# Kernel optimization log

Hardware: AMD Instinct MI355X
Metric: run time of the kernel (lower is better)

Reference implementation:

```python
import jax, jax.numpy as jnp
import numpy as np

B, T, C, H = 2, 2048, 1024, 16
D = C // H  # head_dim = 64


def setup_inputs() -> dict:
    key = jax.random.key(0)
    ks = jax.random.split(key, 5)
    s = 1.0 / np.sqrt(C)
    return {
        "x": jax.random.normal(ks[0], (B, T, C), jnp.float32),
        "Wq": jax.random.normal(ks[1], (C, C), jnp.float32) * s,
        "bq": jnp.zeros((C,), jnp.float32),
        "Wk": jax.random.normal(ks[2], (C, C), jnp.float32) * s,
        "bk": jnp.zeros((C,), jnp.float32),
        "Wv": jax.random.normal(ks[3], (C, C), jnp.float32) * s,
        "bv": jnp.zeros((C,), jnp.float32),
        "Wo": jax.random.normal(ks[4], (C, C), jnp.float32) * s,
        "bo": jnp.zeros((C,), jnp.float32),
    }


def reference(x, Wq, bq, Wk, bk, Wv, bv, Wo, bo):
    Bx, Tx, Cx = x.shape
    # torch Linear: y = x @ W.T + b
    q = (x @ Wq.T + bq).reshape(Bx, Tx, H, D).transpose(0, 2, 1, 3)  # [B,H,T,D]
    k = (x @ Wk.T + bk).reshape(Bx, Tx, H, D).transpose(0, 2, 1, 3)
    v = (x @ Wv.T + bv).reshape(Bx, Tx, H, D).transpose(0, 2, 1, 3)
    att = jnp.einsum("bhqd,bhkd->bhqk", q, k) / np.sqrt(D).astype(np.float32)
    mask = jnp.tril(jnp.ones((Tx, Tx), bool))  # causal mask [T,T]
    att = jnp.where(mask, att, -jnp.inf)
    att = jax.nn.softmax(att, axis=-1)
    out = jnp.einsum("bhqk,bhkd->bhqd", att, v)
    out = out.transpose(0, 2, 1, 3).reshape(Bx, Tx, Cx)
    return out @ Wo.T + bo
```

## Files before the change

kernel.cpp:

```cpp
#include <hip/hip_runtime.h>
#include <hip/hip_bf16.h>

#define B_ 2
#define T_ 2048
#define C_ 1024
#define H_ 16
#define D_ 64

typedef unsigned short u16;
typedef __bf16 bf16x8 __attribute__((ext_vector_type(8)));
typedef float floatx4 __attribute__((ext_vector_type(4)));

__device__ __forceinline__ float bf2f(u16 u) {
  union { unsigned int i; float f; } x; x.i = ((unsigned int)u) << 16; return x.f;
}
__device__ __forceinline__ u16 f2bf(float f) {
  union { float f; unsigned int i; } x; x.f = f;
  unsigned int r = x.i + 0x7fffu + ((x.i >> 16) & 1u);
  return (u16)(r >> 16);
}

__device__ __forceinline__ void gld16(void* lds, const void* g) {
  __builtin_amdgcn_global_load_lds(
      (const __attribute__((address_space(1))) unsigned int*)g,
      (__attribute__((address_space(3))) unsigned int*)lds, 16, 0, 0);
}

#define NXF4 1048576
#define NWF4 262144

__global__ __launch_bounds__(256) void cvt_all(
    const float* __restrict__ x,  const float* __restrict__ Wq,
    const float* __restrict__ Wk, const float* __restrict__ Wv,
    const float* __restrict__ Wo, u16* __restrict__ dst_base)
{
  const int i = blockIdx.x * 256 + threadIdx.x;
  const float* src; size_t off;
  if (i < NXF4)               { src = x;  off = i; }
  else if (i < NXF4 + NWF4)   { src = Wq; off = i - NXF4; }
  else if (i < NXF4 + 2*NWF4) { src = Wk; off = i - (NXF4 + NWF4); }
  else if (i < NXF4 + 3*NWF4) { src = Wv; off = i - (NXF4 + 2*NWF4); }
  else                        { src = Wo; off = i - (NXF4 + 3*NWF4); }
  float4 f = ((const float4*)src)[off];
  ushort4 o;
  o.x = f2bf(f.x); o.y = f2bf(f.y); o.z = f2bf(f.z); o.w = f2bf(f.w);
  ((ushort4*)dst_base)[i] = o;
}

#define QSCALE 0.1803368801111f

__global__ __launch_bounds__(256) void gemm_qkv(
    const u16* __restrict__ X, const u16* __restrict__ Wb,
    const float* __restrict__ b0, const float* __restrict__ b1,
    const float* __restrict__ b2,
    u16* __restrict__ Yq, u16* __restrict__ Yk, u16* __restrict__ Yv)
{
  const int K = C_;
  __shared__ __align__(16) u16 As[128 * 32];
  __shared__ __align__(16) u16 Bs[128 * 32];
  __shared__ __align__(16) u16 Es[64 * 128];

  const int tid  = threadIdx.x;
  const int wv   = tid >> 6;
  const int lane = tid & 63;
  const int mcol = lane & 15;
  const int quad = lane >> 4;
  const int wr = wv >> 1, wc = wv & 1;
  const int m0 = blockIdx.x * 128;
  const int n0 = blockIdx.y * 128;
  const int z  = blockIdx.z;

  const u16* W = Wb + (size_t)z * C_ * C_;
  const float* bias = (z == 0 ? b0 : z == 1 ? b1 : b2);

  const int srow = tid >> 2;
  const int scol = (tid & 3) * 8;
  const u16* xp0 = X + (size_t)(m0 + srow) * K + scol;
  const u16* xp1 = xp0 + (size_t)64 * K;
  const u16* wp0 = W + (size_t)(n0 + srow) * K + scol;
  const u16* wp1 = wp0 + (size_t)64 * K;

  floatx4 acc[4][4] = {};

  for (int k0 = 0; k0 < K; k0 += 32) {
    gld16(&As[tid * 8],        xp0 + k0);
    gld16(&As[2048 + tid * 8], xp1 + k0);
    gld16(&Bs[tid * 8],        wp0 + k0);
    gld16(&Bs[2048 + tid * 8], wp1 + k0);
    __syncthreads();

    bf16x8 a[4], b[4];
#pragma unroll
    for (int rf = 0; rf < 4; ++rf)
      a[rf] = *(const bf16x8*)&As[(wr * 64 + rf * 16 + mcol) * 32 + quad * 8];
#pragma unroll
    for (int cf = 0; cf < 4; ++cf)
      b[cf] = *(const bf16x8*)&Bs[(wc * 64 + cf * 16 + mcol) * 32 + quad * 8];
#pragma unroll
    for (int rf = 0; rf < 4; ++rf)
#pragma unroll
      for (int cf = 0; cf < 4; ++cf)
        acc[rf][cf] = __builtin_amdgcn_mfma_f32_16x16x32_bf16(
            a[rf], b[cf], acc[rf][cf], 0, 0, 0);
    __syncthreads();
  }

  if (z == 2) {
#pragma unroll
    for (int p = 0; p < 2; ++p) {
      __syncthreads();
      if (wc == p) {
#pragma unroll
        for (int cf = 0; cf < 4; ++cf) {
          const int rn = cf * 16 + mcol;
          const float bv = b2[n0 + p * 64 + rn];
#pragma unroll
          for (int rf = 0; rf < 4; ++rf) {
            const int gm = wr * 8 + rf * 2 + (quad >> 1);
            const int slot = gm ^ (rn & 7);
            ushort4 pk;
            pk.x = f2bf(acc[rf][cf][0] + bv);
            pk.y = f2bf(acc[rf][cf][1] + bv);
            pk.z = f2bf(acc[rf][cf][2] + bv);
            pk.w = f2bf(acc[rf][cf][3] + bv);
            *(ushort4*)&Es[rn * 128 + slot * 8 + (quad & 1) * 4] = pk;
          }
        }
      }
      __syncthreads();
      const int c = tid & 15;
      const int bb = m0 >> 11;
      const int t0 = (m0 & (T_ - 1)) + c * 8;
#pragma unroll
      for (int i = 0; i < 4; ++i) {
        const int rn = (tid >> 4) + i * 16;
        const int slot = c ^ (rn & 7);
        const uint4 val = *(const uint4*)&Es[rn * 128 + slot * 8];
        const int n = n0 + p * 64 + rn;
        const int h = n >> 6, d = n & (D_ - 1);
        *(uint4*)&Yv[(((size_t)bb * H_ + h) * D_ + d) * T_ + t0] = val;
      }
    }
  } else {
#pragma unroll
    for (int cf = 0; cf < 4; ++cf) {
      const int n = n0 + wc * 64 + cf * 16 + mcol;
      const float bv = bias[n];
      const int h = n >> 6, d = n & (D_ - 1);
#pragma unroll
      for (int rf = 0; rf < 4; ++rf) {
#pragma unroll
        for (int r = 0; r < 4; ++r) {
          const int m = m0 + wr * 64 + rf * 16 + quad * 4 + r;
          const int bb = m >> 11, t = m & (T_ - 1);
          const float v = acc[rf][cf][r] + bv;
          const size_t idx = (((size_t)bb * H_ + h) * T_ + t) * D_ + d;
          if (z == 0) Yq[idx] = f2bf(v * QSCALE);
          else        Yk[idx] = f2bf(v);
        }
      }
    }
  }
}

__global__ __launch_bounds__(256) void gemm_out(
    const u16* __restrict__ X, const u16* __restrict__ W,
    const float* __restrict__ bias, float* __restrict__ Yf)
{
  const int K = C_, N = C_;
  __shared__ __align__(16) u16 As[128 * 32];
  __shared__ __align__(16) u16 Bs[64 * 32];

  const int tid  = threadIdx.x;
  const int wv   = tid >> 6;
  const int lane = tid & 63;
  const int mcol = lane & 15;
  const int quad = lane >> 4;
  const int wr = wv >> 1, wc = wv & 1;
  const int m0 = blockIdx.x * 128;
  const int n0 = blockIdx.y * 64;

  const int srow = tid >> 2;
  const int scol = (tid & 3) * 8;
  const u16* xp0 = X + (size_t)(m0 + srow) * K + scol;
  const u16* xp1 = xp0 + (size_t)64 * K;
  const u16* wp  = W + (size_t)(n0 + srow) * K + scol;

  floatx4 acc[4][2] = {};

  for (int k0 = 0; k0 < K; k0 += 32) {
    gld16(&As[tid * 8],        xp0 + k0);
    gld16(&As[2048 + tid * 8], xp1 + k0);
    gld16(&Bs[tid * 8],        wp + k0);
    __syncthreads();

    bf16x8 a[4], b[2];
#pragma unroll
    for (int rf = 0; rf < 4; ++rf)
      a[rf] = *(const bf16x8*)&As[(wr * 64 + rf * 16 + mcol) * 32 + quad * 8];
#pragma unroll
    for (int cf = 0; cf < 2; ++cf)
      b[cf] = *(const bf16x8*)&Bs[(wc * 32 + cf * 16 + mcol) * 32 + quad * 8];
#pragma unroll
    for (int rf = 0; rf < 4; ++rf)
#pragma unroll
      for (int cf = 0; cf < 2; ++cf)
        acc[rf][cf] = __builtin_amdgcn_mfma_f32_16x16x32_bf16(
            a[rf], b[cf], acc[rf][cf], 0, 0, 0);
    __syncthreads();
  }

#pragma unroll
  for (int cf = 0; cf < 2; ++cf) {
    const int n = n0 + wc * 32 + cf * 16 + mcol;
    const float bv = bias[n];
#pragma unroll
    for (int rf = 0; rf < 4; ++rf) {
#pragma unroll
      for (int r = 0; r < 4; ++r) {
        const int m = m0 + wr * 64 + rf * 16 + quad * 4 + r;
        Yf[(size_t)m * N + n] = acc[rf][cf][r] + bv;
      }
    }
  }
}

__global__ __launch_bounds__(256) void attn_flash(
    const u16* __restrict__ Q, const u16* __restrict__ K,
    const u16* __restrict__ Vg, u16* __restrict__ O)
{
  __shared__ __align__(16) u16 Ks[64 * 64];
  __shared__ __align__(16) u16 Vt[80 * 64];
  __shared__ __align__(16) u16 Ps[4][16 * 72];

  const int tid  = threadIdx.x;
  const int wv   = tid >> 6;
  const int lane = tid & 63;
  const int mcol = lane & 15;
  const int quad = lane >> 4;

  const int bh = blockIdx.x & 31;
  const int pp = blockIdx.x >> 5;
  const size_t base = (size_t)bh * T_ * D_;
  const int b = bh >> 4, h = bh & (H_ - 1);

  for (int idx = tid; idx < 16 * 64; idx += 256)
    Vt[64 * 64 + idx] = (idx < 64) ? (u16)0x3F80 : (u16)0;

  const int srow = lane >> 3;
  const int sg   = (lane & 7) ^ srow;
  const int c0 = wv * 2, c1 = wv * 2 + 1;
  const int sl0 = (quad ^ (mcol & 7)) * 8;

  const int h3 = mcol >> 3, lo = mcol & 7;
  u16* psw = &Ps[wv][0];
  int colsw[4];
#pragma unroll
  for (int nt = 0; nt < 4; ++nt)
    colsw[nt] = (((nt * 2 + h3) ^ quad) * 8) + lo;
  const int g0 = quad ^ (mcol >> 2);

  for (int half = 0; half < 2; ++half) {
    const int iq = half ? (31 - pp) : pp;

    const u16* qg = Q + base + (size_t)(iq * 64 + wv * 16 + mcol) * D_ + quad * 8;
    const bf16x8 qf0 = *(const bf16x8*)qg;
    const bf16x8 qf1 = *(const bf16x8*)(qg + 32);

    floatx4 oacc[5] = {};

    for (int j = 0; j <= iq; ++j) {
      __syncthreads();
      gld16(&Ks[c0 * 512 + lane * 8],
            K + base + (size_t)(j * 64 + c0 * 8 + srow) * D_ + sg * 8);
      gld16(&Ks[c1 * 512 + lane * 8],
            K + base + (size_t)(j * 64 + c1 * 8 + srow) * D_ + sg * 8);
      gld16(&Vt[c0 * 512 + lane * 8],
            Vg + (size_t)bh * D_ * T_ + (size_t)(c0 * 8 + srow) * T_ + j * 64 + sg * 8);
      gld16(&Vt[c1 * 512 + lane * 8],
            Vg + (size_t)bh * D_ * T_ + (size_t)(c1 * 8 + srow) * T_ + j * 64 + sg * 8);
      __syncthreads();

      floatx4 sacc[4] = {};
#pragma unroll
      for (int nt = 0; nt < 4; ++nt) {
        const u16* kr = &Ks[(nt * 16 + mcol) * 64];
        bf16x8 kb0 = *(const bf16x8*)&kr[sl0];
        bf16x8 kb1 = *(const bf16x8*)&kr[sl0 ^ 32];
        sacc[nt] = __builtin_amdgcn_mfma_f32_16x16x32_bf16(qf0, kb0, sacc[nt], 0, 0, 0);
        sacc[nt] = __builtin_amdgcn_mfma_f32_16x16x32_bf16(qf1, kb1, sacc[nt], 0, 0, 0);
      }

      if (j == iq) {
#pragma unroll
        for (int nt = 0; nt < 4; ++nt) {
          const int col = nt * 16 + mcol;
#pragma unroll
          for (int r = 0; r < 4; ++r)
            if (col > wv * 16 + quad * 4 + r) sacc[nt][r] = -1e30f;
        }
      }

#pragma unroll
      for (int nt = 0; nt < 4; ++nt)
#pragma unroll
        for (int r = 0; r < 4; ++r) {
          const float p = exp2f(sacc[nt][r]);
          psw[(quad * 4 + r) * 72 + colsw[nt]] =
              (u16)((__float_as_uint(p) + 0x8000u) >> 16);
        }

      __builtin_amdgcn_wave_barrier();

      bf16x8 pa0 = *(const bf16x8*)&psw[mcol * 72 + g0 * 8];
      bf16x8 pa1 = *(const bf16x8*)&psw[mcol * 72 + g0 * 8 + 32];
#pragma unroll
      for (int dt = 0; dt < 5; ++dt) {
        const u16* vr = &Vt[(dt * 16 + mcol) * 64];
        bf16x8 vb0 = *(const bf16x8*)&vr[sl0];
        bf16x8 vb1 = *(const bf16x8*)&vr[sl0 ^ 32];
        oacc[dt] = __builtin_amdgcn_mfma_f32_16x16x32_bf16(pa0, vb0, oacc[dt], 0, 0, 0);
        oacc[dt] = __builtin_amdgcn_mfma_f32_16x16x32_bf16(pa1, vb1, oacc[dt], 0, 0, 0);
      }
    }

    float invl[4];
#pragma unroll
    for (int r = 0; r < 4; ++r)
      invl[r] = 1.f / __shfl(oacc[4][r], lane & 48);
#pragma unroll
    for (int dt = 0; dt < 4; ++dt) {
      const int c = h * D_ + dt * 16 + mcol;
#pragma unroll
      for (int r = 0; r < 4; ++r) {
        const int t = iq * 64 + wv * 16 + quad * 4 + r;
        O[((size_t)b * T_ + t) * C_ + c] = f2bf(oacc[dt][r] * invl[r]);
      }
    }
  }
}

extern "C" void kernel_launch(void* const* d_in, const int* in_sizes, int n_in,
                              void* d_out, int out_size, void* d_ws, size_t ws_size,
                              hipStream_t stream) {
  const float* x  = (const float*)d_in[0];
  const float* Wq = (const float*)d_in[1];
  const float* bq = (const float*)d_in[2];
  const float* Wk = (const float*)d_in[3];
  const float* bk = (const float*)d_in[4];
  const float* Wv = (const float*)d_in[5];
  const float* bv = (const float*)d_in[6];
  const float* Wo = (const float*)d_in[7];
  const float* bo = (const float*)d_in[8];
  float* out = (float*)d_out;

  const size_t NX = (size_t)B_ * T_ * C_;
  const size_t NW = (size_t)C_ * C_;

  u16* xb  = (u16*)d_ws;
  u16* wqb = xb  + NX;
  u16* wkb = wqb + NW;
  u16* wvb = wkb + NW;
  u16* wob = wvb + NW;
  u16* q   = wob + NW;
  u16* k   = q   + NX;
  u16* v   = k   + NX;
  u16* ctx = v   + NX;

  cvt_all<<<dim3((NXF4 + 4 * NWF4) / 256), 256, 0, stream>>>(x, Wq, Wk, Wv, Wo, xb);

  gemm_qkv<<<dim3(32, 8, 3), 256, 0, stream>>>(xb, wqb, bq, bk, bv, q, k, v);

  attn_flash<<<dim3(512), 256, 0, stream>>>(q, k, v, ctx);

  gemm_out<<<dim3(32, 16), 256, 0, stream>>>(ctx, wob, bo, out);
}
```

Before: 202.1 us.

## Double GEMM K-tile depth and split attention into one query tile per block

Both GEMMs now stage a K-slice of 64 instead of 32 per iteration, which halves the number of barrier pairs per output tile at the cost of twice the LDS per block. The attention kernel no longer pairs a light and a heavy query tile per block; it launches 1024 blocks, each handling a single query tile, with the tile index derived so that heavy and light tiles are interleaved in launch order. This gives more parallelism but relies on the hardware scheduler rather than explicit pairing to balance the causal work.

```diff
diff --git a/kernel.cpp b/kernel.cpp
--- a/kernel.cpp
+++ b/kernel.cpp
@@ -56,8 +56,8 @@
     u16* __restrict__ Yq, u16* __restrict__ Yk, u16* __restrict__ Yv)
 {
   const int K = C_;
-  __shared__ __align__(16) u16 As[128 * 32];
-  __shared__ __align__(16) u16 Bs[128 * 32];
+  __shared__ __align__(16) u16 As[128 * 64];
+  __shared__ __align__(16) u16 Bs[128 * 64];
   __shared__ __align__(16) u16 Es[64 * 128];
 
   const int tid  = threadIdx.x;
@@ -71,37 +71,38 @@
   const int z  = blockIdx.z;
 
   const u16* W = Wb + (size_t)z * C_ * C_;
-  const float* bias = (z == 0 ? b0 : z == 1 ? b1 : b2);
-
-  const int srow = tid >> 2;
-  const int scol = (tid & 3) * 8;
-  const u16* xp0 = X + (size_t)(m0 + srow) * K + scol;
-  const u16* xp1 = xp0 + (size_t)64 * K;
-  const u16* wp0 = W + (size_t)(n0 + srow) * K + scol;
-  const u16* wp1 = wp0 + (size_t)64 * K;
+
+  const int srow = tid >> 3;
+  const int sgr  = (tid & 7) * 8;
+  const u16* xp = X + (size_t)(m0 + srow) * K + sgr;
+  const u16* wp = W + (size_t)(n0 + srow) * K + sgr;
 
   floatx4 acc[4][4] = {};
 
-  for (int k0 = 0; k0 < K; k0 += 32) {
-    gld16(&As[tid * 8],        xp0 + k0);
-    gld16(&As[2048 + tid * 8], xp1 + k0);
-    gld16(&Bs[tid * 8],        wp0 + k0);
-    gld16(&Bs[2048 + tid * 8], wp1 + k0);
-    __syncthreads();
-
-    bf16x8 a[4], b[4];
-#pragma unroll
-    for (int rf = 0; rf < 4; ++rf)
-      a[rf] = *(const bf16x8*)&As[(wr * 64 + rf * 16 + mcol) * 32 + quad * 8];
-#pragma unroll
-    for (int cf = 0; cf < 4; ++cf)
-      b[cf] = *(const bf16x8*)&Bs[(wc * 64 + cf * 16 + mcol) * 32 + quad * 8];
-#pragma unroll
-    for (int rf = 0; rf < 4; ++rf)
+  for (int k0 = 0; k0 < K; k0 += 64) {
+#pragma unroll
+    for (int c = 0; c < 4; ++c) {
+      gld16(&As[c * 2048 + tid * 8], xp + (size_t)(c * 32) * K + k0);
+      gld16(&Bs[c * 2048 + tid * 8], wp + (size_t)(c * 32) * K + k0);
+    }
+    __syncthreads();
+
+#pragma unroll
+    for (int kk = 0; kk < 2; ++kk) {
+      bf16x8 a[4], b[4];
+#pragma unroll
+      for (int rf = 0; rf < 4; ++rf)
+        a[rf] = *(const bf16x8*)&As[(wr * 64 + rf * 16 + mcol) * 64 + kk * 32 + quad * 8];
 #pragma unroll
       for (int cf = 0; cf < 4; ++cf)
-        acc[rf][cf] = __builtin_amdgcn_mfma_f32_16x16x32_bf16(
-            a[rf], b[cf], acc[rf][cf], 0, 0, 0);
+        b[cf] = *(const bf16x8*)&Bs[(wc * 64 + cf * 16 + mcol) * 64 + kk * 32 + quad * 8];
+#pragma unroll
+      for (int rf = 0; rf < 4; ++rf)
+#pragma unroll
+        for (int cf = 0; cf < 4; ++cf)
+          acc[rf][cf] = __builtin_amdgcn_mfma_f32_16x16x32_bf16(
+              a[rf], b[cf], acc[rf][cf], 0, 0, 0);
+    }
     __syncthreads();
   }
 
@@ -142,6 +143,7 @@
       }
     }
   } else {
+    const float* bias = (z == 0 ? b0 : b1);
 #pragma unroll
     for (int cf = 0; cf < 4; ++cf) {
       const int n = n0 + wc * 64 + cf * 16 + mcol;
@@ -168,8 +170,8 @@
     const float* __restrict__ bias, float* __restrict__ Yf)
 {
   const int K = C_, N = C_;
-  __shared__ __align__(16) u16 As[128 * 32];
-  __shared__ __align__(16) u16 Bs[64 * 32];
+  __shared__ __align__(16) u16 As[128 * 64];
+  __shared__ __align__(16) u16 Bs[64 * 64];
 
   const int tid  = threadIdx.x;
   const int wv   = tid >> 6;
@@ -180,33 +182,38 @@
   const int m0 = blockIdx.x * 128;
   const int n0 = blockIdx.y * 64;
 
-  const int srow = tid >> 2;
-  const int scol = (tid & 3) * 8;
-  const u16* xp0 = X + (size_t)(m0 + srow) * K + scol;
-  const u16* xp1 = xp0 + (size_t)64 * K;
-  const u16* wp  = W + (size_t)(n0 + srow) * K + scol;
+  const int srow = tid >> 3;
+  const int sgr  = (tid & 7) * 8;
+  const u16* xp = X + (size_t)(m0 + srow) * K + sgr;
+  const u16* wp = W + (size_t)(n0 + srow) * K + sgr;
 
   floatx4 acc[4][2] = {};
 
-  for (int k0 = 0; k0 < K; k0 += 32) {
-    gld16(&As[tid * 8],        xp0 + k0);
-    gld16(&As[2048 + tid * 8], xp1 + k0);
-    gld16(&Bs[tid * 8],        wp + k0);
-    __syncthreads();
-
-    bf16x8 a[4], b[2];
-#pragma unroll
-    for (int rf = 0; rf < 4; ++rf)
-      a[rf] = *(const bf16x8*)&As[(wr * 64 + rf * 16 + mcol) * 32 + quad * 8];
-#pragma unroll
-    for (int cf = 0; cf < 2; ++cf)
-      b[cf] = *(const bf16x8*)&Bs[(wc * 32 + cf * 16 + mcol) * 32 + quad * 8];
-#pragma unroll
-    for (int rf = 0; rf < 4; ++rf)
+  for (int k0 = 0; k0 < K; k0 += 64) {
+#pragma unroll
+    for (int c = 0; c < 4; ++c)
+      gld16(&As[c * 2048 + tid * 8], xp + (size_t)(c * 32) * K + k0);
+#pragma unroll
+    for (int c = 0; c < 2; ++c)
+      gld16(&Bs[c * 2048 + tid * 8], wp + (size_t)(c * 32) * K + k0);
+    __syncthreads();
+
+#pragma unroll
+    for (int kk = 0; kk < 2; ++kk) {
+      bf16x8 a[4], b[2];
+#pragma unroll
+      for (int rf = 0; rf < 4; ++rf)
+        a[rf] = *(const bf16x8*)&As[(wr * 64 + rf * 16 + mcol) * 64 + kk * 32 + quad * 8];
 #pragma unroll
       for (int cf = 0; cf < 2; ++cf)
-        acc[rf][cf] = __builtin_amdgcn_mfma_f32_16x16x32_bf16(
-            a[rf], b[cf], acc[rf][cf], 0, 0, 0);
+        b[cf] = *(const bf16x8*)&Bs[(wc * 32 + cf * 16 + mcol) * 64 + kk * 32 + quad * 8];
+#pragma unroll
+      for (int rf = 0; rf < 4; ++rf)
+#pragma unroll
+        for (int cf = 0; cf < 2; ++cf)
+          acc[rf][cf] = __builtin_amdgcn_mfma_f32_16x16x32_bf16(
+              a[rf], b[cf], acc[rf][cf], 0, 0, 0);
+    }
     __syncthreads();
   }
 
@@ -239,8 +246,9 @@
   const int mcol = lane & 15;
   const int quad = lane >> 4;
 
-  const int bh = blockIdx.x & 31;
-  const int pp = blockIdx.x >> 5;
+  const int bx = blockIdx.x;
+  const int iq = (bx & 3) * 8 + (bx >> 7);
+  const int bh = (bx >> 2) & 31;
   const size_t base = (size_t)bh * T_ * D_;
   const int b = bh >> 4, h = bh & (H_ - 1);
 
@@ -260,82 +268,78 @@
     colsw[nt] = (((nt * 2 + h3) ^ quad) * 8) + lo;
   const int g0 = quad ^ (mcol >> 2);
 
-  for (int half = 0; half < 2; ++half) {
-    const int iq = half ? (31 - pp) : pp;
-
-    const u16* qg = Q + base + (size_t)(iq * 64 + wv * 16 + mcol) * D_ + quad * 8;
-    const bf16x8 qf0 = *(const bf16x8*)qg;
-    const bf16x8 qf1 = *(const bf16x8*)(qg + 32);
-
-    floatx4 oacc[5] = {};
-
-    for (int j = 0; j <= iq; ++j) {
-      __syncthreads();
-      gld16(&Ks[c0 * 512 + lane * 8],
-            K + base + (size_t)(j * 64 + c0 * 8 + srow) * D_ + sg * 8);
-      gld16(&Ks[c1 * 512 + lane * 8],
-            K + base + (size_t)(j * 64 + c1 * 8 + srow) * D_ + sg * 8);
-      gld16(&Vt[c0 * 512 + lane * 8],
-            Vg + (size_t)bh * D_ * T_ + (size_t)(c0 * 8 + srow) * T_ + j * 64 + sg * 8);
-      gld16(&Vt[c1 * 512 + lane * 8],
-            Vg + (size_t)bh * D_ * T_ + (size_t)(c1 * 8 + srow) * T_ + j * 64 + sg * 8);
-      __syncthreads();
-
-      floatx4 sacc[4] = {};
+  const u16* qg = Q + base + (size_t)(iq * 64 + wv * 16 + mcol) * D_ + quad * 8;
+  const bf16x8 qf0 = *(const bf16x8*)qg;
+  const bf16x8 qf1 = *(const bf16x8*)(qg + 32);
+
+  floatx4 oacc[5] = {};
+
+  for (int j = 0; j <= iq; ++j) {
+    __syncthreads();
+    gld16(&Ks[c0 * 512 + lane * 8],
+          K + base + (size_t)(j * 64 + c0 * 8 + srow) * D_ + sg * 8);
+    gld16(&Ks[c1 * 512 + lane * 8],
+          K + base + (size_t)(j * 64 + c1 * 8 + srow) * D_ + sg * 8);
+    gld16(&Vt[c0 * 512 + lane * 8],
+          Vg + (size_t)bh * D_ * T_ + (size_t)(c0 * 8 + srow) * T_ + j * 64 + sg * 8);
+    gld16(&Vt[c1 * 512 + lane * 8],
+          Vg + (size_t)bh * D_ * T_ + (size_t)(c1 * 8 + srow) * T_ + j * 64 + sg * 8);
+    __syncthreads();
+
+    floatx4 sacc[4] = {};
+#pragma unroll
+    for (int nt = 0; nt < 4; ++nt) {
+      const u16* kr = &Ks[(nt * 16 + mcol) * 64];
+      bf16x8 kb0 = *(const bf16x8*)&kr[sl0];
+      bf16x8 kb1 = *(const bf16x8*)&kr[sl0 ^ 32];
+      sacc[nt] = __builtin_amdgcn_mfma_f32_16x16x32_bf16(qf0, kb0, sacc[nt], 0, 0, 0);
+      sacc[nt] = __builtin_amdgcn_mfma_f32_16x16x32_bf16(qf1, kb1, sacc[nt], 0, 0, 0);
+    }
+
+    if (j == iq) {
 #pragma unroll
       for (int nt = 0; nt < 4; ++nt) {
-        const u16* kr = &Ks[(nt * 16 + mcol) * 64];
-        bf16x8 kb0 = *(const bf16x8*)&kr[sl0];
-        bf16x8 kb1 = *(const bf16x8*)&kr[sl0 ^ 32];
-        sacc[nt] = __builtin_amdgcn_mfma_f32_16x16x32_bf16(qf0, kb0, sacc[nt], 0, 0, 0);
-        sacc[nt] = __builtin_amdgcn_mfma_f32_16x16x32_bf16(qf1, kb1, sacc[nt], 0, 0, 0);
-      }
-
-      if (j == iq) {
-#pragma unroll
-        for (int nt = 0; nt < 4; ++nt) {
-          const int col = nt * 16 + mcol;
-#pragma unroll
-          for (int r = 0; r < 4; ++r)
-            if (col > wv * 16 + quad * 4 + r) sacc[nt][r] = -1e30f;
-        }
-      }
-
-#pragma unroll
-      for (int nt = 0; nt < 4; ++nt)
-#pragma unroll
-        for (int r = 0; r < 4; ++r) {
-          const float p = exp2f(sacc[nt][r]);
-          psw[(quad * 4 + r) * 72 + colsw[nt]] =
-              (u16)((__float_as_uint(p) + 0x8000u) >> 16);
-        }
-
-      __builtin_amdgcn_wave_barrier();
-
-      bf16x8 pa0 = *(const bf16x8*)&psw[mcol * 72 + g0 * 8];
-      bf16x8 pa1 = *(const bf16x8*)&psw[mcol * 72 + g0 * 8 + 32];
-#pragma unroll
-      for (int dt = 0; dt < 5; ++dt) {
-        const u16* vr = &Vt[(dt * 16 + mcol) * 64];
-        bf16x8 vb0 = *(const bf16x8*)&vr[sl0];
-        bf16x8 vb1 = *(const bf16x8*)&vr[sl0 ^ 32];
-        oacc[dt] = __builtin_amdgcn_mfma_f32_16x16x32_bf16(pa0, vb0, oacc[dt], 0, 0, 0);
-        oacc[dt] = __builtin_amdgcn_mfma_f32_16x16x32_bf16(pa1, vb1, oacc[dt], 0, 0, 0);
-      }
-    }
-
-    float invl[4];
-#pragma unroll
-    for (int r = 0; r < 4; ++r)
-      invl[r] = 1.f / __shfl(oacc[4][r], lane & 48);
-#pragma unroll
-    for (int dt = 0; dt < 4; ++dt) {
-      const int c = h * D_ + dt * 16 + mcol;
+        const int col = nt * 16 + mcol;
+#pragma unroll
+        for (int r = 0; r < 4; ++r)
+          if (col > wv * 16 + quad * 4 + r) sacc[nt][r] = -1e30f;
+      }
+    }
+
+#pragma unroll
+    for (int nt = 0; nt < 4; ++nt)
 #pragma unroll
       for (int r = 0; r < 4; ++r) {
-        const int t = iq * 64 + wv * 16 + quad * 4 + r;
-        O[((size_t)b * T_ + t) * C_ + c] = f2bf(oacc[dt][r] * invl[r]);
-      }
+        const float p = exp2f(sacc[nt][r]);
+        psw[(quad * 4 + r) * 72 + colsw[nt]] =
+            (u16)((__float_as_uint(p) + 0x8000u) >> 16);
+      }
+
+    __builtin_amdgcn_wave_barrier();
+
+    bf16x8 pa0 = *(const bf16x8*)&psw[mcol * 72 + g0 * 8];
+    bf16x8 pa1 = *(const bf16x8*)&psw[mcol * 72 + g0 * 8 + 32];
+#pragma unroll
+    for (int dt = 0; dt < 5; ++dt) {
+      const u16* vr = &Vt[(dt * 16 + mcol) * 64];
+      bf16x8 vb0 = *(const bf16x8*)&vr[sl0];
+      bf16x8 vb1 = *(const bf16x8*)&vr[sl0 ^ 32];
+      oacc[dt] = __builtin_amdgcn_mfma_f32_16x16x32_bf16(pa0, vb0, oacc[dt], 0, 0, 0);
+      oacc[dt] = __builtin_amdgcn_mfma_f32_16x16x32_bf16(pa1, vb1, oacc[dt], 0, 0, 0);
+    }
+  }
+
+  float invl[4];
+#pragma unroll
+  for (int r = 0; r < 4; ++r)
+    invl[r] = 1.f / __shfl(oacc[4][r], lane & 48);
+#pragma unroll
+  for (int dt = 0; dt < 4; ++dt) {
+    const int c = h * D_ + dt * 16 + mcol;
+#pragma unroll
+    for (int r = 0; r < 4; ++r) {
+      const int t = iq * 64 + wv * 16 + quad * 4 + r;
+      O[((size_t)b * T_ + t) * C_ + c] = f2bf(oacc[dt][r] * invl[r]);
     }
   }
 }
@@ -371,7 +375,7 @@
 
   gemm_qkv<<<dim3(32, 8, 3), 256, 0, stream>>>(xb, wqb, bq, bk, bv, q, k, v);
 
-  attn_flash<<<dim3(512), 256, 0, stream>>>(q, k, v, ctx);
+  attn_flash<<<dim3(1024), 256, 0, stream>>>(q, k, v, ctx);
 
   gemm_out<<<dim3(32, 16), 256, 0, stream>>>(ctx, wob, bo, out);
 }
```

Result: slower. 239.1 us (+18.3%).

## Double-buffer K/V tiles in flash attention to prefetch the next block

Applied to the files above, without the earlier changes.

The attention kernel now keeps two LDS buffers for the K and V^T tiles. It issues the async global-to-LDS load for tile j+1 before computing on tile j, and drops one of the two barriers per iteration. The goal is to hide global load latency behind the MFMA and softmax work. In exchange, LDS use per block roughly doubles, which may lower occupancy. Overlap only happens if the compiler's wait on the async LDS loads is not conservative, since a wait on all outstanding loads before the LDS reads would also stall on the prefetch. A minor bias-pointer move in the projection kernel is incidental.

```diff
diff --git a/kernel.cpp b/kernel.cpp
--- a/kernel.cpp
+++ b/kernel.cpp
@@ -71,7 +71,6 @@
   const int z  = blockIdx.z;
 
   const u16* W = Wb + (size_t)z * C_ * C_;
-  const float* bias = (z == 0 ? b0 : z == 1 ? b1 : b2);
 
   const int srow = tid >> 2;
   const int scol = (tid & 3) * 8;
@@ -142,6 +141,7 @@
       }
     }
   } else {
+    const float* bias = (z == 0 ? b0 : b1);
 #pragma unroll
     for (int cf = 0; cf < 4; ++cf) {
       const int n = n0 + wc * 64 + cf * 16 + mcol;
@@ -225,12 +225,15 @@
   }
 }
 
+#define KSB 4096
+#define VTB 5120
+
 __global__ __launch_bounds__(256) void attn_flash(
     const u16* __restrict__ Q, const u16* __restrict__ K,
     const u16* __restrict__ Vg, u16* __restrict__ O)
 {
-  __shared__ __align__(16) u16 Ks[64 * 64];
-  __shared__ __align__(16) u16 Vt[80 * 64];
+  __shared__ __align__(16) u16 Ks[2 * KSB];
+  __shared__ __align__(16) u16 Vt[2 * VTB];
   __shared__ __align__(16) u16 Ps[4][16 * 72];
 
   const int tid  = threadIdx.x;
@@ -241,11 +244,15 @@
 
   const int bh = blockIdx.x & 31;
   const int pp = blockIdx.x >> 5;
-  const size_t base = (size_t)bh * T_ * D_;
+  const size_t base  = (size_t)bh * T_ * D_;
+  const size_t vbase = (size_t)bh * D_ * T_;
   const int b = bh >> 4, h = bh & (H_ - 1);
 
-  for (int idx = tid; idx < 16 * 64; idx += 256)
-    Vt[64 * 64 + idx] = (idx < 64) ? (u16)0x3F80 : (u16)0;
+  for (int idx = tid; idx < 16 * 64; idx += 256) {
+    const u16 val = (idx < 64) ? (u16)0x3F80 : (u16)0;
+    Vt[64 * 64 + idx]       = val;
+    Vt[VTB + 64 * 64 + idx] = val;
+  }
 
   const int srow = lane >> 3;
   const int sg   = (lane & 7) ^ srow;
@@ -260,6 +267,11 @@
     colsw[nt] = (((nt * 2 + h3) ^ quad) * 8) + lo;
   const int g0 = quad ^ (mcol >> 2);
 
+  const size_t koff0 = base + (size_t)(c0 * 8 + srow) * D_ + sg * 8;
+  const size_t koff1 = base + (size_t)(c1 * 8 + srow) * D_ + sg * 8;
+  const size_t voff0 = vbase + (size_t)(c0 * 8 + srow) * T_ + sg * 8;
+  const size_t voff1 = vbase + (size_t)(c1 * 8 + srow) * T_ + sg * 8;
+
   for (int half = 0; half < 2; ++half) {
     const int iq = half ? (31 - pp) : pp;
 
@@ -269,22 +281,33 @@
 
     floatx4 oacc[5] = {};
 
+    __syncthreads();
+    gld16(&Ks[c0 * 512 + lane * 8], K  + koff0);
+    gld16(&Ks[c1 * 512 + lane * 8], K  + koff1);
+    gld16(&Vt[c0 * 512 + lane * 8], Vg + voff0);
+    gld16(&Vt[c1 * 512 + lane * 8], Vg + voff1);
+
     for (int j = 0; j <= iq; ++j) {
+      const int cur = j & 1;
       __syncthreads();
-      gld16(&Ks[c0 * 512 + lane * 8],
-            K + base + (size_t)(j * 64 + c0 * 8 + srow) * D_ + sg * 8);
-      gld16(&Ks[c1 * 512 + lane * 8],
-            K + base + (size_t)(j * 64 + c1 * 8 + srow) * D_ + sg * 8);
-      gld16(&Vt[c0 * 512 + lane * 8],
-            Vg + (size_t)bh * D_ * T_ + (size_t)(c0 * 8 + srow) * T_ + j * 64 + sg * 8);
-      gld16(&Vt[c1 * 512 + lane * 8],
-            Vg + (size_t)bh * D_ * T_ + (size_t)(c1 * 8 + srow) * T_ + j * 64 + sg * 8);
-      __syncthreads();
+
+      if (j < iq) {
+        const int nb = cur ^ 1;
+        const size_t kj = (size_t)(j + 1) * 64 * D_;
+        const int    vj = (j + 1) * 64;
+        gld16(&Ks[nb * KSB + c0 * 512 + lane * 8], K  + koff0 + kj);
+        gld16(&Ks[nb * KSB + c1 * 512 + lane * 8], K  + koff1 + kj);
+        gld16(&Vt[nb * VTB + c0 * 512 + lane * 8], Vg + voff0 + vj);
+        gld16(&Vt[nb * VTB + c1 * 512 + lane * 8], Vg + voff1 + vj);
+      }
+
+      const u16* ksb = &Ks[cur * KSB];
+      const u16* vtb = &Vt[cur * VTB];
 
       floatx4 sacc[4] = {};
 #pragma unroll
       for (int nt = 0; nt < 4; ++nt) {
-        const u16* kr = &Ks[(nt * 16 + mcol) * 64];
+        const u16* kr = &ksb[(nt * 16 + mcol) * 64];
         bf16x8 kb0 = *(const bf16x8*)&kr[sl0];
         bf16x8 kb1 = *(const bf16x8*)&kr[sl0 ^ 32];
         sacc[nt] = __builtin_amdgcn_mfma_f32_16x16x32_bf16(qf0, kb0, sacc[nt], 0, 0, 0);
@@ -316,7 +339,7 @@
       bf16x8 pa1 = *(const bf16x8*)&psw[mcol * 72 + g0 * 8 + 32];
 #pragma unroll
       for (int dt = 0; dt < 5; ++dt) {
-        const u16* vr = &Vt[(dt * 16 + mcol) * 64];
+        const u16* vr = &vtb[(dt * 16 + mcol) * 64];
         bf16x8 vb0 = *(const bf16x8*)&vr[sl0];
         bf16x8 vb1 = *(const bf16x8*)&vr[sl0 ^ 32];
         oacc[dt] = __builtin_amdgcn_mfma_f32_16x16x32_bf16(pa0, vb0, oacc[dt], 0, 0, 0);
```

After: 199.1 us. No clear change (-1.5%).
